# Kernel tuning notes

Hardware: AMD Instinct MI355X
Metric: run time of the kernel (lower is better)

## Reference

```python
import jax, jax.numpy as jnp
import numpy as np

N, E = 50000, 800000          # nodes, directed edges
IN_DIM, HC, OUT_DIM = 128, 64, 128
NEG_SLOPE = 0.2               # PyG GATConv default leaky_relu slope
EPS = 1e-5                    # PyG LayerNorm default eps


def setup_inputs() -> dict:
    key = jax.random.key(0)
    ks = jax.random.split(key, 10)
    s = 0.1
    return {
        "x": jax.random.normal(ks[0], (N, IN_DIM), jnp.float32),
        "edge_index": jax.random.randint(ks[1], (2, E), 0, N, dtype=jnp.int32),
        # conv1: GATConv(IN_DIM -> HC, heads=2, concat=True)
        "W1": jax.random.normal(ks[2], (IN_DIM, 2 * HC), jnp.float32) * s,
        "att_src1": jax.random.normal(ks[3], (2, HC), jnp.float32) * s,
        "att_dst1": jax.random.normal(ks[4], (2, HC), jnp.float32) * s,
        "b1": jnp.zeros((2 * HC,), jnp.float32),
        "ln1_w": jnp.ones((2 * HC,), jnp.float32),
        "ln1_b": jnp.zeros((2 * HC,), jnp.float32),
        # conv2: GATConv(2*HC -> OUT_DIM, heads=1, concat=False)
        "W2": jax.random.normal(ks[5], (2 * HC, OUT_DIM), jnp.float32) * s,
        "att_src2": jax.random.normal(ks[6], (1, OUT_DIM), jnp.float32) * s,
        "att_dst2": jax.random.normal(ks[7], (1, OUT_DIM), jnp.float32) * s,
        "b2": jnp.zeros((OUT_DIM,), jnp.float32),
        "ln2_w": jnp.ones((OUT_DIM,), jnp.float32),
        "ln2_b": jnp.zeros((OUT_DIM,), jnp.float32),
    }


def gat_conv(x, src, dst, W, att_src, att_dst, bias, heads, C, concat):
    """PyG GATConv (shared lin for src/dst, self-loops already in src/dst)."""
    n = x.shape[0]
    h = (x @ W).reshape(n, heads, C)                       # [N,H,C]
    a_src = jnp.einsum('nhc,hc->nh', h, att_src)           # [N,H]
    a_dst = jnp.einsum('nhc,hc->nh', h, att_dst)           # [N,H]
    e = jax.nn.leaky_relu(a_src[src] + a_dst[dst], NEG_SLOPE)   # [E',H]
    # numerically-stable softmax over incoming edges of each dst node
    emax = jax.ops.segment_max(e, dst, num_segments=n)     # [N,H] (self-loops => non-empty)
    ex = jnp.exp(e - emax[dst])
    denom = jax.ops.segment_sum(ex, dst, num_segments=n)
    alpha = ex / (denom[dst] + 1e-16)                      # [E',H]
    out = jax.ops.segment_sum(h[src] * alpha[:, :, None], dst, num_segments=n)  # [N,H,C]
    out = out.reshape(n, heads * C) if concat else out.mean(axis=1)
    return out + bias


def graph_layernorm(x, w, b):
    """PyG LayerNorm, mode='graph', single graph: normalize over ALL nodes+features."""
    mean = x.mean()
    xc = x - mean
    var = (xc * xc).mean()
    return xc * jax.lax.rsqrt(var + EPS) * w + b


def reference(x, edge_index, W1, att_src1, att_dst1, b1, ln1_w, ln1_b,
              W2, att_src2, att_dst2, b2, ln2_w, ln2_b):
    n = x.shape[0]
    loop = jnp.arange(n, dtype=edge_index.dtype)
    src = jnp.concatenate([edge_index[0], loop])           # add self-loops for GAT convs
    dst = jnp.concatenate([edge_index[1], loop])

    h = gat_conv(x, src, dst, W1, att_src1, att_dst1, b1, heads=2, C=HC, concat=True)
    h = jax.nn.relu(graph_layernorm(h, ln1_w, ln1_b))
    h = gat_conv(h, src, dst, W2, att_src2, att_dst2, b2, heads=1, C=OUT_DIM, concat=False)
    h = graph_layernorm(h, ln2_w, ln2_b)

    # SimpleConv(aggr='mean') over the ORIGINAL edges (no self-loops), then residual
    s0, d0 = edge_index[0], edge_index[1]
    agg = jax.ops.segment_sum(h[s0], d0, num_segments=n)
    cnt = jax.ops.segment_sum(jnp.ones(s0.shape, h.dtype), d0, num_segments=n)
    mean_agg = agg / jnp.maximum(cnt, 1.0)[:, None]
    return jax.nn.relu(mean_agg + x)
```

## Files before the change

kernel.cpp:

```cpp
#include <hip/hip_runtime.h>
#include <hip/hip_bf16.h>
#include <cstdint>
#include <cstddef>

#define NN 50000
#define EE 800000
#define DD 128
#define NEG 0.2f
#define EPSL 1e-5f

#define NB   196
#define EPB  4096
#define NBKT 196
#define HM   (NBKT * NB)

#define GROWS 64
#define AB    (NN / 8)

typedef __hip_bfloat16 bf16;
typedef short short8 __attribute__((ext_vector_type(8)));
typedef float f32x4 __attribute__((ext_vector_type(4)));

__device__ inline float bflo(unsigned u) { return __uint_as_float(u << 16); }
__device__ inline float bfhi(unsigned u) { return __uint_as_float(u & 0xffff0000u); }
__device__ inline float bf2f(unsigned short u) { return __uint_as_float((unsigned)u << 16); }

__device__ inline unsigned short f2bf(float f) {
    __bf16 h = (__bf16)f;
    return __builtin_bit_cast(unsigned short, h);
}
__device__ inline unsigned pack2(float a, float b) {
    return (unsigned)f2bf(a) | ((unsigned)f2bf(b) << 16);
}

__device__ inline void store4(float* Out, size_t idx, float4 v) {
    *(float4*)&Out[idx] = v;
}
__device__ inline void store4(bf16* Out, size_t idx, float4 v) {
    union { bf16 b[4]; ushort4 u; } cv;
    cv.b[0] = (bf16)v.x; cv.b[1] = (bf16)v.y; cv.b[2] = (bf16)v.z; cv.b[3] = (bf16)v.w;
    *(ushort4*)&Out[idx] = cv.u;
}


__global__ __launch_bounds__(256) void hist_kernel(const int* __restrict__ ei,
                                                   int* __restrict__ histG) {
    __shared__ int lh[NBKT];
    int tid = threadIdx.x;
    for (int t = tid; t < NBKT; t += 256) lh[t] = 0;
    __syncthreads();
    int base = blockIdx.x * EPB;
    #pragma unroll
    for (int j = 0; j < EPB / 1024; ++j) {
        int i4 = base + (j * 256 + tid) * 4;
        if (i4 < EE) {
            int4 d4 = *(const int4*)&ei[EE + i4];
            atomicAdd(&lh[(unsigned)d4.x >> 8], 1);
            atomicAdd(&lh[(unsigned)d4.y >> 8], 1);
            atomicAdd(&lh[(unsigned)d4.z >> 8], 1);
            atomicAdd(&lh[(unsigned)d4.w >> 8], 1);
        }
    }
    __syncthreads();
    for (int t = tid; t < NBKT; t += 256) histG[t * NB + blockIdx.x] = lh[t];
}

__global__ __launch_bounds__(1024) void scan_hist_kernel(const int* __restrict__ histG,
                                                         int* __restrict__ offs,
                                                         int* __restrict__ bstart) {
    __shared__ int wsum[16];
    __shared__ int carry_s;
    int tid = threadIdx.x, lane = tid & 63, wv = tid >> 6;
    if (tid == 0) carry_s = 0;
    __syncthreads();
    for (int base = 0; base < HM; base += 4096) {
        int i4 = base + tid * 4;
        int4 v = make_int4(0, 0, 0, 0);
        if (i4 + 3 < HM) v = *(const int4*)&histG[i4];
        else {
            if (i4 + 0 < HM) v.x = histG[i4 + 0];
            if (i4 + 1 < HM) v.y = histG[i4 + 1];
            if (i4 + 2 < HM) v.z = histG[i4 + 2];
            if (i4 + 3 < HM) v.w = histG[i4 + 3];
        }
        int tsum = v.x + v.y + v.z + v.w;
        int x = tsum;
        for (int off = 1; off < 64; off <<= 1) {
            int t = __shfl_up(x, off);
            if (lane >= off) x += t;
        }
        if (lane == 63) wsum[wv] = x;
        __syncthreads();
        if (wv == 0) {
            int s = (lane < 16) ? wsum[lane] : 0;
            for (int off = 1; off < 16; off <<= 1) {
                int t = __shfl_up(s, off);
                if (lane >= off) s += t;
            }
            if (lane < 16) wsum[lane] = s;
        }
        __syncthreads();
        int waveoff = (wv == 0) ? 0 : wsum[wv - 1];
        int carry = carry_s;
        int o0 = carry + waveoff + x - tsum;
        int o1 = o0 + v.x, o2 = o1 + v.y, o3 = o2 + v.z;
        if (i4 + 3 < HM) *(int4*)&offs[i4] = make_int4(o0, o1, o2, o3);
        else {
            if (i4 + 0 < HM) offs[i4 + 0] = o0;
            if (i4 + 1 < HM) offs[i4 + 1] = o1;
            if (i4 + 2 < HM) offs[i4 + 2] = o2;
            if (i4 + 3 < HM) offs[i4 + 3] = o3;
        }
        if (i4 < HM && (i4 % NB) == 0) bstart[i4 / NB] = o0;
        __syncthreads();
        if (tid == 0) carry_s += wsum[15];
        __syncthreads();
    }
    if (tid == 0) bstart[NBKT] = carry_s;
}

__global__ __launch_bounds__(256) void bucket_sort_kernel(const unsigned* __restrict__ tmp,
                                                          const int* __restrict__ bstart,
                                                          unsigned* __restrict__ col,
                                                          int* __restrict__ row_ptr) {
    __shared__ int cnt[256];
    __shared__ int cpos[256];
    __shared__ int wtot[4];
    int tid = threadIdx.x, lane = tid & 63, wv = tid >> 6;
    int s0 = bstart[blockIdx.x], s1 = bstart[blockIdx.x + 1];
    cnt[tid] = 0;
    __syncthreads();
    for (int i = s0 + tid; i < s1; i += 256)
        atomicAdd(&cnt[(tmp[i] >> 16) & 0xFF], 1);
    __syncthreads();
    int v = cnt[tid];
    int x = v;
    for (int off = 1; off < 64; off <<= 1) {
        int t = __shfl_up(x, off);
        if (lane >= off) x += t;
    }
    if (lane == 63) wtot[wv] = x;
    __syncthreads();
    int add = 0;
    for (int k = 0; k < wv; ++k) add += wtot[k];
    int start = s0 + add + x - v;
    cpos[tid] = start;
    int d = blockIdx.x * 256 + tid;
    if (d <= NN) row_ptr[d] = start;
    __syncthreads();
    for (int i = s0 + tid; i < s1; i += 256) {
        unsigned key = tmp[i];
        int pos = atomicAdd(&cpos[(key >> 16) & 0xFF], 1);
        col[pos] = key;
    }
}

template <int H, bool LN, typename XT>
__device__ __forceinline__ void gemm_attn_body(int gb,
                                               const XT* __restrict__ X,
                                               const float* __restrict__ W,
                                               const float* __restrict__ att_s,
                                               const float* __restrict__ att_d,
                                               const double* __restrict__ stats,
                                               const float* __restrict__ lnw,
                                               const float* __restrict__ lnb,
                                               bf16* __restrict__ Hout,
                                               float* __restrict__ a_src,
                                               float* __restrict__ a_dst) {
    __shared__ __align__(16) char lds[(128 * 136 + 64 * 136) * 2 + 2048];
    unsigned short* Bt = (unsigned short*)lds;
    unsigned short* As = (unsigned short*)(lds + 128 * 136 * 2);
    float* Cs = (float*)lds;
    float* psum = (float*)(lds + (128 * 136 + 64 * 136) * 2);

    int tid = threadIdx.x;
    int row0 = gb * GROWS;

    {
        int c = tid & 127, kg = tid >> 7;
        #pragma unroll 2
        for (int i = 0; i < 8; ++i) {
            int k0 = i * 16 + kg * 4;
            float wa = W[(size_t)(k0 + 0) * DD + c];
            float wb = W[(size_t)(k0 + 1) * DD + c];
            float wcv = W[(size_t)(k0 + 2) * DD + c];
            float wdv = W[(size_t)(k0 + 3) * DD + c];
            uint2 pk = make_uint2(pack2(wa, wb), pack2(wcv, wdv));
            *(uint2*)&Bt[c * 136 + k0] = pk;
        }
    }
    {
        int sub = tid & 31, rq = tid >> 5;
        int c4 = sub * 4;
        float mean = 0.f, inv = 1.f;
        float4 lw4 = make_float4(1.f, 1.f, 1.f, 1.f), lb4 = make_float4(0.f, 0.f, 0.f, 0.f);
        if (LN) {
            const double M = (double)NN * DD;
            double mean_d = stats[0] / M;
            double var_d = stats[1] / M - mean_d * mean_d;
            mean = (float)mean_d;
            inv = rsqrtf((float)var_d + EPSL);
            lw4 = *(const float4*)&lnw[c4];
            lb4 = *(const float4*)&lnb[c4];
        }
        #pragma unroll
        for (int i = 0; i < 4; ++i) {
            int r = i * 16 + rq;
            int row = row0 + r;
            float4 xv = make_float4(0.f, 0.f, 0.f, 0.f);
            if (row < NN) {
                if constexpr (sizeof(XT) == 4) {
                    xv = *(const float4*)&((const float*)X)[(size_t)row * DD + c4];
                } else {
                    ushort4 xb = *(const ushort4*)&((const unsigned short*)X)[(size_t)row * DD + c4];
                    xv = make_float4(bf2f(xb.x), bf2f(xb.y), bf2f(xb.z), bf2f(xb.w));
                }
            }
            if (LN) {
                xv.x = fmaxf((xv.x - mean) * inv * lw4.x + lb4.x, 0.f);
                xv.y = fmaxf((xv.y - mean) * inv * lw4.y + lb4.y, 0.f);
                xv.z = fmaxf((xv.z - mean) * inv * lw4.z + lb4.z, 0.f);
                xv.w = fmaxf((xv.w - mean) * inv * lw4.w + lb4.w, 0.f);
            }
            uint2 pk = make_uint2(pack2(xv.x, xv.y), pack2(xv.z, xv.w));
            *(uint2*)&As[r * 136 + c4] = pk;
        }
    }
    __syncthreads();

    int lane = tid & 63, w = tid >> 6;
    int rg = w & 3, cg = w >> 2;
    int l15 = lane & 15, quad = lane >> 4;
    f32x4 acc[4];
    #pragma unroll
    for (int t = 0; t < 4; ++t) acc[t] = 0.f;
    const unsigned short* Arow = As + (rg * 16 + l15) * 136 + quad * 8;
    const unsigned short* Brow = Bt + l15 * 136 + quad * 8;
    #pragma unroll
    for (int ks = 0; ks < 4; ++ks) {
        short8 a = *(const short8*)(Arow + ks * 32);
        #pragma unroll
        for (int tt = 0; tt < 4; ++tt) {
            short8 b = *(const short8*)(Brow + (cg * 4 + tt) * 16 * 136 + ks * 32);
            acc[tt] = __builtin_amdgcn_mfma_f32_16x16x32_bf16(a, b, acc[tt], 0, 0, 0);
        }
    }
    __syncthreads();

    #pragma unroll
    for (int tt = 0; tt < 4; ++tt)
        #pragma unroll
        for (int r = 0; r < 4; ++r)
            Cs[(rg * 16 + quad * 4 + r) * 132 + (cg * 4 + tt) * 16 + l15] = acc[tt][r];

    float ds[4] = {0.f, 0.f, 0.f, 0.f}, dd[4] = {0.f, 0.f, 0.f, 0.f};
    #pragma unroll
    for (int tt = 0; tt < 4; ++tt) {
        int cc = (cg * 4 + tt) * 16 + l15;
        float as_ = att_s[cc], ad_ = att_d[cc];
        #pragma unroll
        for (int r = 0; r < 4; ++r) {
            ds[r] = fmaf(acc[tt][r], as_, ds[r]);
            dd[r] = fmaf(acc[tt][r], ad_, dd[r]);
        }
    }
    #pragma unroll
    for (int off = 1; off < 16; off <<= 1) {
        #pragma unroll
        for (int r = 0; r < 4; ++r) {
            ds[r] += __shfl_xor(ds[r], off);
            dd[r] += __shfl_xor(dd[r], off);
        }
    }
    if (l15 == 0) {
        #pragma unroll
        for (int r = 0; r < 4; ++r) {
            int rr = rg * 16 + quad * 4 + r;
            int row = row0 + rr;
            if (H == 2) {
                if (row < NN) {
                    a_src[row * 2 + cg] = ds[r];
                    a_dst[row * 2 + cg] = dd[r];
                }
            } else {
                psum[cg * 64 + rr] = ds[r];
                psum[128 + cg * 64 + rr] = dd[r];
            }
        }
    }
    __syncthreads();

    if (H == 1 && tid < 64) {
        int row = row0 + tid;
        if (row < NN) {
            a_src[row] = psum[tid] + psum[64 + tid];
            a_dst[row] = psum[128 + tid] + psum[192 + tid];
        }
    }

    {
        int sub = tid & 31, rq = tid >> 5;
        int c4 = sub * 4;
        unsigned short* Hp = (unsigned short*)Hout;
        #pragma unroll
        for (int i = 0; i < 4; ++i) {
            int r = i * 16 + rq;
            int row = row0 + r;
            if (row < NN) {
                float4 cv = *(const float4*)&Cs[r * 132 + c4];
                ushort4 pk;
                pk.x = f2bf(cv.x); pk.y = f2bf(cv.y);
                pk.z = f2bf(cv.z); pk.w = f2bf(cv.w);
                *(ushort4*)&Hp[(size_t)row * DD + c4] = pk;
            }
        }
    }
}

template <int H, bool LN, typename XT>
__global__ __launch_bounds__(512) void gemm_attn(const XT* __restrict__ X,
                                                 const float* __restrict__ W,
                                                 const float* __restrict__ att_s,
                                                 const float* __restrict__ att_d,
                                                 const double* __restrict__ stats,
                                                 const float* __restrict__ lnw,
                                                 const float* __restrict__ lnb,
                                                 bf16* __restrict__ Hout,
                                                 float* __restrict__ a_src,
                                                 float* __restrict__ a_dst) {
    gemm_attn_body<H, LN, XT>(blockIdx.x, X, W, att_s, att_d, stats, lnw, lnb,
                              Hout, a_src, a_dst);
}

__global__ __launch_bounds__(512) void scatter_gemm1(const int* __restrict__ ei,
                                                     const int* __restrict__ offs,
                                                     unsigned* __restrict__ tmp,
                                                     const float* __restrict__ X,
                                                     const float* __restrict__ W,
                                                     const float* __restrict__ att_s,
                                                     const float* __restrict__ att_d,
                                                     bf16* __restrict__ Hout,
                                                     float* __restrict__ a_src,
                                                     float* __restrict__ a_dst) {
    if (blockIdx.x < NB) {
        __shared__ int lofs[NBKT];
        int tid = threadIdx.x;
        for (int t = tid; t < NBKT; t += 512) lofs[t] = offs[t * NB + blockIdx.x];
        __syncthreads();
        int base = blockIdx.x * EPB;
        #pragma unroll
        for (int j = 0; j < EPB / 2048; ++j) {
            int i4 = base + (j * 512 + tid) * 4;
            if (i4 < EE) {
                int4 s4 = *(const int4*)&ei[i4];
                int4 d4 = *(const int4*)&ei[EE + i4];
                unsigned k0 = ((unsigned)d4.x << 16) | (unsigned)s4.x;
                unsigned k1 = ((unsigned)d4.y << 16) | (unsigned)s4.y;
                unsigned k2 = ((unsigned)d4.z << 16) | (unsigned)s4.z;
                unsigned k3 = ((unsigned)d4.w << 16) | (unsigned)s4.w;
                tmp[atomicAdd(&lofs[(unsigned)d4.x >> 8], 1)] = k0;
                tmp[atomicAdd(&lofs[(unsigned)d4.y >> 8], 1)] = k1;
                tmp[atomicAdd(&lofs[(unsigned)d4.z >> 8], 1)] = k2;
                tmp[atomicAdd(&lofs[(unsigned)d4.w >> 8], 1)] = k3;
            }
        }
    } else {
        gemm_attn_body<2, false, float>(blockIdx.x - NB, X, W, att_s, att_d,
                                        nullptr, nullptr, nullptr, Hout, a_src, a_dst);
    }
}

template <int H, typename OT>
__global__ __launch_bounds__(256) void gat_agg(const int* __restrict__ row_ptr,
                                               const unsigned* __restrict__ col,
                                               const bf16* __restrict__ Hin,
                                               const float* __restrict__ a_src,
                                               const float* __restrict__ a_dst,
                                               const float* __restrict__ bias,
                                               OT* __restrict__ Out,
                                               float2* __restrict__ pstats) {
    int tid = threadIdx.x;
    int sl = tid & 31;
    int hw = tid >> 5;
    int n = blockIdx.x * 8 + hw;
    int c0 = sl * 4;
    const int head4 = (H == 2) ? (sl >> 4) : 0;

    int beg = row_ptr[n], end = row_ptr[n + 1];
    int deg = end - beg;

    float ad0 = a_dst[n * H + 0];
    float ad1 = (H == 2) ? a_dst[n * H + 1] : 0.f;
    const ushort* Hp = (const ushort*)Hin + c0;

    float acc[4] = {0.f, 0.f, 0.f, 0.f};
    float dl0 = 0.f, dl1 = 0.f;

    for (int base = 0; base < deg; base += 32) {
        int ecnt = min(32, deg - base);
        int sv = 0; float w0v = 0.f, w1v = 0.f;
        if (sl < ecnt) {
            sv = (int)(col[beg + base + sl] & 0xffffu);
            if (H == 2) {
                float2 av = *(const float2*)&a_src[sv * 2];
                float e0 = av.x + ad0; e0 = (e0 > 0.f) ? e0 : NEG * e0;
                float e1 = av.y + ad1; e1 = (e1 > 0.f) ? e1 : NEG * e1;
                w0v = __expf(e0); w1v = __expf(e1);
                dl0 += w0v; dl1 += w1v;
            } else {
                float e0 = a_src[sv] + ad0; e0 = (e0 > 0.f) ? e0 : NEG * e0;
                w0v = __expf(e0);
                dl0 += w0v;
            }
        }
        int j = 0;
        for (; j + 7 < ecnt; j += 8) {
            int s[8]; float ww[8];
            uint2 h[8];
            #pragma unroll
            for (int u = 0; u < 8; ++u) {
                s[u] = __shfl(sv, j + u, 32);
                if (H == 2) {
                    float a0 = __shfl(w0v, j + u, 32), b0 = __shfl(w1v, j + u, 32);
                    ww[u] = head4 ? b0 : a0;
                } else {
                    ww[u] = __shfl(w0v, j + u, 32);
                }
            }
            #pragma unroll
            for (int u = 0; u < 8; ++u) h[u] = *(const uint2*)(Hp + (size_t)s[u] * DD);
            #pragma unroll
            for (int u = 0; u < 8; ++u) {
                acc[0] = fmaf(ww[u], bflo(h[u].x), acc[0]);
                acc[1] = fmaf(ww[u], bfhi(h[u].x), acc[1]);
                acc[2] = fmaf(ww[u], bflo(h[u].y), acc[2]);
                acc[3] = fmaf(ww[u], bfhi(h[u].y), acc[3]);
            }
        }
        for (; j < ecnt; ++j) {
            int s = __shfl(sv, j, 32);
            float w;
            if (H == 2) {
                float a0 = __shfl(w0v, j, 32), b0 = __shfl(w1v, j, 32);
                w = head4 ? b0 : a0;
            } else {
                w = __shfl(w0v, j, 32);
            }
            uint2 hv = *(const uint2*)(Hp + (size_t)s * DD);
            acc[0] = fmaf(w, bflo(hv.x), acc[0]); acc[1] = fmaf(w, bfhi(hv.x), acc[1]);
            acc[2] = fmaf(w, bflo(hv.y), acc[2]); acc[3] = fmaf(w, bfhi(hv.y), acc[3]);
        }
    }

    #pragma unroll
    for (int off = 1; off < 32; off <<= 1) {
        dl0 += __shfl_xor(dl0, off);
        if (H == 2) dl1 += __shfl_xor(dl1, off);
    }

    float e0 = a_src[n * H + 0] + ad0; e0 = (e0 > 0.f) ? e0 : NEG * e0;
    float ws0 = __expf(e0);
    float ws1 = 0.f;
    if (H == 2) {
        float e1 = a_src[n * H + 1] + ad1; e1 = (e1 > 0.f) ? e1 : NEG * e1;
        ws1 = __expf(e1);
    }
    float den = (H == 2 && head4) ? (dl1 + ws1) : (dl0 + ws0);
    float wself = (H == 2 && head4) ? ws1 : ws0;
    float rinv = 1.f / (den + 1e-16f);
    uint2 hs = *(const uint2*)(Hp + (size_t)n * DD);
    float4 bi = *(const float4*)&bias[c0];
    float4 o;
    o.x = fmaf(wself, bflo(hs.x), acc[0]) * rinv + bi.x;
    o.y = fmaf(wself, bfhi(hs.x), acc[1]) * rinv + bi.y;
    o.z = fmaf(wself, bflo(hs.y), acc[2]) * rinv + bi.z;
    o.w = fmaf(wself, bfhi(hs.y), acc[3]) * rinv + bi.w;
    store4(Out, (size_t)n * DD + c0, o);

    float t1 = o.x + o.y + o.z + o.w;
    float t2 = o.x * o.x + o.y * o.y + o.z * o.z + o.w * o.w;
    #pragma unroll
    for (int off = 1; off < 32; off <<= 1) {
        t1 += __shfl_xor(t1, off);
        t2 += __shfl_xor(t2, off);
    }
    __shared__ float2 ps[8];
    if (sl == 0) ps[hw] = make_float2(t1, t2);
    __syncthreads();
    if (tid == 0) {
        float a = 0.f, b = 0.f;
        #pragma unroll
        for (int k = 0; k < 8; ++k) { a += ps[k].x; b += ps[k].y; }
        pstats[blockIdx.x] = make_float2(a, b);
    }
}

__global__ __launch_bounds__(1024) void reduce_stats_kernel(const float2* __restrict__ pstats,
                                                            double* __restrict__ stats) {
    int tid = threadIdx.x, lane = tid & 63, wv = tid >> 6;
    double s1 = 0.0, s2 = 0.0;
    for (int i = tid; i < AB; i += 1024) {
        float2 v = pstats[i];
        s1 += (double)v.x; s2 += (double)v.y;
    }
    for (int off = 32; off; off >>= 1) {
        s1 += __shfl_xor(s1, off);
        s2 += __shfl_xor(s2, off);
    }
    __shared__ double w1[16], w2[16];
    if (lane == 0) { w1[wv] = s1; w2[wv] = s2; }
    __syncthreads();
    if (tid == 0) {
        double a = 0.0, b = 0.0;
        for (int i = 0; i < 16; ++i) { a += w1[i]; b += w2[i]; }
        stats[0] = a; stats[1] = b;
    }
}

__global__ __launch_bounds__(256) void simpleconv_kernel(const int* __restrict__ row_ptr,
                                                         const unsigned* __restrict__ col,
                                                         const bf16* __restrict__ Hin,
                                                         const float* __restrict__ X,
                                                         const double* __restrict__ stats,
                                                         const float* __restrict__ lnw,
                                                         const float* __restrict__ lnb,
                                                         float* __restrict__ Out) {
    int tid = threadIdx.x;
    int sl = tid & 31;
    int n = blockIdx.x * 8 + (tid >> 5);
    int c0 = sl * 4;
    int beg = row_ptr[n], end = row_ptr[n + 1];
    int deg = end - beg;
    const ushort* Hp = (const ushort*)Hin + c0;

    float acc[4] = {0.f, 0.f, 0.f, 0.f};
    for (int base = 0; base < deg; base += 32) {
        int ecnt = min(32, deg - base);
        int sv = 0;
        if (sl < ecnt) sv = (int)(col[beg + base + sl] & 0xffffu);
        int j = 0;
        for (; j + 7 < ecnt; j += 8) {
            int s[8]; uint2 h[8];
            #pragma unroll
            for (int u = 0; u < 8; ++u) s[u] = __shfl(sv, j + u, 32);
            #pragma unroll
            for (int u = 0; u < 8; ++u) h[u] = *(const uint2*)(Hp + (size_t)s[u] * DD);
            #pragma unroll
            for (int u = 0; u < 8; ++u) {
                acc[0] += bflo(h[u].x); acc[1] += bfhi(h[u].x);
                acc[2] += bflo(h[u].y); acc[3] += bfhi(h[u].y);
            }
        }
        for (; j < ecnt; ++j) {
            int s = __shfl(sv, j, 32);
            uint2 hv = *(const uint2*)(Hp + (size_t)s * DD);
            acc[0] += bflo(hv.x); acc[1] += bfhi(hv.x);
            acc[2] += bflo(hv.y); acc[3] += bfhi(hv.y);
        }
    }

    const double M = (double)NN * DD;
    double mean_d = stats[0] / M;
    double var_d = stats[1] / M - mean_d * mean_d;
    float mean2 = (float)mean_d;
    float inv2 = rsqrtf((float)var_d + EPSL);
    float rc = 1.f / (float)((deg > 0) ? deg : 1);
    float4 xr = *(const float4*)&X[(size_t)n * DD + c0];
    float4 o;
    if (deg > 0) {
        float4 lw = *(const float4*)&lnw[c0];
        float4 lb = *(const float4*)&lnb[c0];
        o.x = (acc[0] * rc - mean2) * inv2 * lw.x + lb.x;
        o.y = (acc[1] * rc - mean2) * inv2 * lw.y + lb.y;
        o.z = (acc[2] * rc - mean2) * inv2 * lw.z + lb.z;
        o.w = (acc[3] * rc - mean2) * inv2 * lw.w + lb.w;
    } else {
        o.x = o.y = o.z = o.w = 0.f;
    }
    o.x = fmaxf(o.x + xr.x, 0.f);
    o.y = fmaxf(o.y + xr.y, 0.f);
    o.z = fmaxf(o.z + xr.z, 0.f);
    o.w = fmaxf(o.w + xr.w, 0.f);
    *(float4*)&Out[(size_t)n * DD + c0] = o;
}

extern "C" void kernel_launch(void* const* d_in, const int* in_sizes, int n_in,
                              void* d_out, int out_size, void* d_ws, size_t ws_size,
                              hipStream_t stream) {
    const float* x    = (const float*)d_in[0];
    const int*   ei   = (const int*)d_in[1];
    const float* W1   = (const float*)d_in[2];
    const float* as1  = (const float*)d_in[3];
    const float* ad1  = (const float*)d_in[4];
    const float* b1   = (const float*)d_in[5];
    const float* ln1w = (const float*)d_in[6];
    const float* ln1b = (const float*)d_in[7];
    const float* W2   = (const float*)d_in[8];
    const float* as2  = (const float*)d_in[9];
    const float* ad2  = (const float*)d_in[10];
    const float* b2   = (const float*)d_in[11];
    const float* ln2w = (const float*)d_in[12];
    const float* ln2b = (const float*)d_in[13];
    float* out = (float*)d_out;

    char* p = (char*)d_ws;
    auto alloc = [&](size_t bytes) {
        void* r = (void*)p;
        p += (bytes + 255) & ~(size_t)255;
        return r;
    };
    unsigned* tmp     = (unsigned*)alloc((size_t)EE * 4);
    unsigned* col     = (unsigned*)alloc((size_t)EE * 4);
    int*      histG   = (int*)alloc((size_t)HM * 4);
    int*      offs    = (int*)alloc((size_t)HM * 4);
    int*      bstart  = (int*)alloc((size_t)(NBKT + 1) * 4);
    int*      row_ptr = (int*)alloc((size_t)(NN + 256) * 4);
    double*   stats1  = (double*)alloc(16);
    double*   stats2  = (double*)alloc(16);
    float2*   pstats  = (float2*)alloc((size_t)AB * 8);
    bf16*     bufA    = (bf16*)alloc((size_t)NN * DD * 2);
    bf16*     bufB    = (bf16*)alloc((size_t)NN * DD * 2);
    float*    aS1     = (float*)alloc((size_t)NN * 2 * 4);
    float*    aD1     = (float*)alloc((size_t)NN * 2 * 4);
    float*    aS2     = (float*)alloc((size_t)NN * 4);
    float*    aD2     = (float*)alloc((size_t)NN * 4);

    const int GB = (NN + GROWS - 1) / GROWS;

    hist_kernel<<<NB, 256, 0, stream>>>(ei, histG);
    scan_hist_kernel<<<1, 1024, 0, stream>>>(histG, offs, bstart);
    scatter_gemm1<<<NB + GB, 512, 0, stream>>>(ei, offs, tmp,
                                               x, W1, as1, ad1, bufA, aS1, aD1);
    bucket_sort_kernel<<<NBKT, 256, 0, stream>>>(tmp, bstart, col, row_ptr);

    gat_agg<2, bf16><<<AB, 256, 0, stream>>>(row_ptr, col, bufA, aS1, aD1, b1, bufB, pstats);
    reduce_stats_kernel<<<1, 1024, 0, stream>>>(pstats, stats1);

    gemm_attn<1, true, bf16><<<GB, 512, 0, stream>>>(bufB, W2, as2, ad2,
                                                     stats1, ln1w, ln1b,
                                                     bufA, aS2, aD2);
    gat_agg<1, bf16><<<AB, 256, 0, stream>>>(row_ptr, col, bufA, aS2, aD2, b2, bufB, pstats);
    reduce_stats_kernel<<<1, 1024, 0, stream>>>(pstats, stats2);

    simpleconv_kernel<<<AB, 256, 0, stream>>>(row_ptr, col, bufB, x,
                                              stats2, ln2w, ln2b, out);
}
```

Measured before the change: 270.1 us.

## Stage bucket sort in LDS and fold layer-1 stats reduction into GEMM

```diff
diff --git a/kernel.cpp b/kernel.cpp
--- a/kernel.cpp
+++ b/kernel.cpp
@@ -13,6 +13,7 @@
 #define EPB  4096
 #define NBKT 196
 #define HM   (NBKT * NB)
+#define SCAP 7168
 
 #define GROWS 64
 #define AB    (NN / 8)
@@ -119,39 +120,66 @@
     if (tid == 0) bstart[NBKT] = carry_s;
 }
 
-__global__ __launch_bounds__(256) void bucket_sort_kernel(const unsigned* __restrict__ tmp,
+__global__ __launch_bounds__(512) void bucket_sort_kernel(const unsigned* __restrict__ tmp,
                                                           const int* __restrict__ bstart,
                                                           unsigned* __restrict__ col,
                                                           int* __restrict__ row_ptr) {
     __shared__ int cnt[256];
     __shared__ int cpos[256];
     __shared__ int wtot[4];
+    __shared__ unsigned stage[SCAP];
+    __shared__ unsigned sorted[SCAP];
     int tid = threadIdx.x, lane = tid & 63, wv = tid >> 6;
     int s0 = bstart[blockIdx.x], s1 = bstart[blockIdx.x + 1];
-    cnt[tid] = 0;
-    __syncthreads();
-    for (int i = s0 + tid; i < s1; i += 256)
-        atomicAdd(&cnt[(tmp[i] >> 16) & 0xFF], 1);
-    __syncthreads();
-    int v = cnt[tid];
-    int x = v;
-    for (int off = 1; off < 64; off <<= 1) {
-        int t = __shfl_up(x, off);
-        if (lane >= off) x += t;
-    }
-    if (lane == 63) wtot[wv] = x;
-    __syncthreads();
-    int add = 0;
-    for (int k = 0; k < wv; ++k) add += wtot[k];
-    int start = s0 + add + x - v;
-    cpos[tid] = start;
-    int d = blockIdx.x * 256 + tid;
-    if (d <= NN) row_ptr[d] = start;
-    __syncthreads();
-    for (int i = s0 + tid; i < s1; i += 256) {
-        unsigned key = tmp[i];
-        int pos = atomicAdd(&cpos[(key >> 16) & 0xFF], 1);
-        col[pos] = key;
+    int cntE = s1 - s0;
+    bool lds_ok = (cntE <= SCAP);
+    for (int t = tid; t < 256; t += 512) cnt[t] = 0;
+    __syncthreads();
+    if (lds_ok) {
+        for (int i = tid; i < cntE; i += 512) {
+            unsigned k = tmp[s0 + i];
+            stage[i] = k;
+            atomicAdd(&cnt[(k >> 16) & 0xFF], 1);
+        }
+    } else {
+        for (int i = s0 + tid; i < s1; i += 512)
+            atomicAdd(&cnt[(tmp[i] >> 16) & 0xFF], 1);
+    }
+    __syncthreads();
+    int v = 0, x = 0;
+    if (tid < 256) {
+        v = cnt[tid];
+        x = v;
+        for (int off = 1; off < 64; off <<= 1) {
+            int t = __shfl_up(x, off);
+            if (lane >= off) x += t;
+        }
+        if (lane == 63) wtot[wv] = x;
+    }
+    __syncthreads();
+    if (tid < 256) {
+        int add = 0;
+        for (int k = 0; k < wv; ++k) add += wtot[k];
+        int start = s0 + add + x - v;
+        cpos[tid] = start;
+        int d = blockIdx.x * 256 + tid;
+        if (d <= NN) row_ptr[d] = start;
+    }
+    __syncthreads();
+    if (lds_ok) {
+        for (int i = tid; i < cntE; i += 512) {
+            unsigned key = stage[i];
+            int pos = atomicAdd(&cpos[(key >> 16) & 0xFF], 1);
+            sorted[pos - s0] = key;
+        }
+        __syncthreads();
+        for (int i = tid; i < cntE; i += 512) col[s0 + i] = sorted[i];
+    } else {
+        for (int i = s0 + tid; i < s1; i += 512) {
+            unsigned key = tmp[i];
+            int pos = atomicAdd(&cpos[(key >> 16) & 0xFF], 1);
+            col[pos] = key;
+        }
     }
 }
 
@@ -161,7 +189,7 @@
                                                const float* __restrict__ W,
                                                const float* __restrict__ att_s,
                                                const float* __restrict__ att_d,
-                                               const double* __restrict__ stats,
+                                               const float2* __restrict__ pstats,
                                                const float* __restrict__ lnw,
                                                const float* __restrict__ lnb,
                                                bf16* __restrict__ Hout,
@@ -172,9 +200,19 @@
     unsigned short* As = (unsigned short*)(lds + 128 * 136 * 2);
     float* Cs = (float*)lds;
     float* psum = (float*)(lds + (128 * 136 + 64 * 136) * 2);
+    __shared__ double w1d[8], w2d[8], sred[2];
 
     int tid = threadIdx.x;
+    int lane = tid & 63, w = tid >> 6;
     int row0 = gb * GROWS;
+
+    double s1 = 0.0, s2 = 0.0;
+    if (LN) {
+        for (int i = tid; i < AB; i += 512) {
+            float2 pv = pstats[i];
+            s1 += (double)pv.x; s2 += (double)pv.y;
+        }
+    }
 
     {
         int c = tid & 127, kg = tid >> 7;
@@ -189,6 +227,24 @@
             *(uint2*)&Bt[c * 136 + k0] = pk;
         }
     }
+
+    if (LN) {
+        #pragma unroll
+        for (int off = 32; off; off >>= 1) {
+            s1 += __shfl_xor(s1, off);
+            s2 += __shfl_xor(s2, off);
+        }
+        if (lane == 0) { w1d[w] = s1; w2d[w] = s2; }
+    }
+    __syncthreads();
+    if (LN && tid == 0) {
+        double a = 0.0, b = 0.0;
+        #pragma unroll
+        for (int k = 0; k < 8; ++k) { a += w1d[k]; b += w2d[k]; }
+        sred[0] = a; sred[1] = b;
+    }
+    __syncthreads();
+
     {
         int sub = tid & 31, rq = tid >> 5;
         int c4 = sub * 4;
@@ -196,8 +252,8 @@
         float4 lw4 = make_float4(1.f, 1.f, 1.f, 1.f), lb4 = make_float4(0.f, 0.f, 0.f, 0.f);
         if (LN) {
             const double M = (double)NN * DD;
-            double mean_d = stats[0] / M;
-            double var_d = stats[1] / M - mean_d * mean_d;
+            double mean_d = sred[0] / M;
+            double var_d = sred[1] / M - mean_d * mean_d;
             mean = (float)mean_d;
             inv = rsqrtf((float)var_d + EPSL);
             lw4 = *(const float4*)&lnw[c4];
@@ -228,7 +284,6 @@
     }
     __syncthreads();
 
-    int lane = tid & 63, w = tid >> 6;
     int rg = w & 3, cg = w >> 2;
     int l15 = lane & 15, quad = lane >> 4;
     f32x4 acc[4];
@@ -322,13 +377,13 @@
                                                  const float* __restrict__ W,
                                                  const float* __restrict__ att_s,
                                                  const float* __restrict__ att_d,
-                                                 const double* __restrict__ stats,
+                                                 const float2* __restrict__ pstats,
                                                  const float* __restrict__ lnw,
                                                  const float* __restrict__ lnb,
                                                  bf16* __restrict__ Hout,
                                                  float* __restrict__ a_src,
                                                  float* __restrict__ a_dst) {
-    gemm_attn_body<H, LN, XT>(blockIdx.x, X, W, att_s, att_d, stats, lnw, lnb,
+    gemm_attn_body<H, LN, XT>(blockIdx.x, X, W, att_s, att_d, pstats, lnw, lnb,
                               Hout, a_src, a_dst);
 }
 
@@ -615,7 +670,6 @@
     int*      offs    = (int*)alloc((size_t)HM * 4);
     int*      bstart  = (int*)alloc((size_t)(NBKT + 1) * 4);
     int*      row_ptr = (int*)alloc((size_t)(NN + 256) * 4);
-    double*   stats1  = (double*)alloc(16);
     double*   stats2  = (double*)alloc(16);
     float2*   pstats  = (float2*)alloc((size_t)AB * 8);
     bf16*     bufA    = (bf16*)alloc((size_t)NN * DD * 2);
@@ -631,13 +685,12 @@
     scan_hist_kernel<<<1, 1024, 0, stream>>>(histG, offs, bstart);
     scatter_gemm1<<<NB + GB, 512, 0, stream>>>(ei, offs, tmp,
                                                x, W1, as1, ad1, bufA, aS1, aD1);
-    bucket_sort_kernel<<<NBKT, 256, 0, stream>>>(tmp, bstart, col, row_ptr);
+    bucket_sort_kernel<<<NBKT, 512, 0, stream>>>(tmp, bstart, col, row_ptr);
 
     gat_agg<2, bf16><<<AB, 256, 0, stream>>>(row_ptr, col, bufA, aS1, aD1, b1, bufB, pstats);
-    reduce_stats_kernel<<<1, 1024, 0, stream>>>(pstats, stats1);
 
     gemm_attn<1, true, bf16><<<GB, 512, 0, stream>>>(bufB, W2, as2, ad2,
-                                                     stats1, ln1w, ln1b,
+                                                     pstats, ln1w, ln1b,
                                                      bufA, aS2, aD2);
     gat_agg<1, bf16><<<AB, 256, 0, stream>>>(row_ptr, col, bufA, aS2, aD2, b2, bufB, pstats);
     reduce_stats_kernel<<<1, 1024, 0, stream>>>(pstats, stats2);
```

After: 266.5 us. About the same (-1.3%).
